# Performance work log

Hardware: AMD Instinct MI355X
Metric: run time of the kernel (lower is better)

The kernel has to match this reference:

```python
import jax, jax.numpy as jnp
import numpy as np

HIDDEN = 2048
NUM_HEADS = 16
HEAD_DIM = HIDDEN // NUM_HEADS
INTER = 8192
EPS = 1e-6


def setup_inputs() -> dict:
    key = jax.random.key(0)
    ks = jax.random.split(key, 10)
    s = 0.02
    return {
        "x": jax.random.normal(ks[0], (2, 2048, HIDDEN), dtype=jnp.float32),
        "w_ln1": jnp.ones((HIDDEN,), dtype=jnp.float32),
        "wq": jax.random.normal(ks[1], (HIDDEN, HIDDEN), dtype=jnp.float32) * s,
        "wk": jax.random.normal(ks[2], (HIDDEN, HIDDEN), dtype=jnp.float32) * s,
        "wv": jax.random.normal(ks[3], (HIDDEN, HIDDEN), dtype=jnp.float32) * s,
        "wo": jax.random.normal(ks[4], (HIDDEN, HIDDEN), dtype=jnp.float32) * s,
        "w_ln2": jnp.ones((HIDDEN,), dtype=jnp.float32),
        "wg": jax.random.normal(ks[5], (INTER, HIDDEN), dtype=jnp.float32) * s,
        "wu": jax.random.normal(ks[6], (INTER, HIDDEN), dtype=jnp.float32) * s,
        "wd": jax.random.normal(ks[7], (HIDDEN, INTER), dtype=jnp.float32) * s,
    }


def rmsnorm(x, w):
    rms = jnp.sqrt(jnp.mean(x * x, axis=-1, keepdims=True) + EPS)
    return x / rms * w


def attention(x, wq, wk, wv, wo):
    B, T, C = x.shape
    # weights are [out, in] (torch Linear convention) -> x @ W.T
    q = (x @ wq.T).reshape(B, T, NUM_HEADS, HEAD_DIM)
    k = (x @ wk.T).reshape(B, T, NUM_HEADS, HEAD_DIM)
    v = (x @ wv.T).reshape(B, T, NUM_HEADS, HEAD_DIM)
    scores = jnp.einsum("bqhd,bkhd->bhqk", q, k) / jnp.sqrt(jnp.float32(HEAD_DIM))
    attn = jax.nn.softmax(scores, axis=-1)
    out = jnp.einsum("bhqk,bkhd->bqhd", attn, v).reshape(B, T, C)
    return out @ wo.T


def mlp(x, wg, wu, wd):
    return (jax.nn.silu(x @ wg.T) * (x @ wu.T)) @ wd.T


def reference(x, w_ln1, wq, wk, wv, wo, w_ln2, wg, wu, wd):
    x = x + attention(rmsnorm(x, w_ln1), wq, wk, wv, wo)
    x = x + mlp(rmsnorm(x, w_ln2), wg, wu, wd)
    return x
```

## Files before the change

### kernel.cpp

```cpp
#include <hip/hip_runtime.h>
#include <stdint.h>

typedef unsigned short u16;
typedef unsigned int   u32;
typedef short s16x8 __attribute__((ext_vector_type(8)));
typedef u16   u16x8 __attribute__((ext_vector_type(8)));
typedef u32   u32x4 __attribute__((ext_vector_type(4)));
typedef float f32x4 __attribute__((ext_vector_type(4)));

__device__ __forceinline__ u16 f2bf(float f) {
    u32 u = __float_as_uint(f);
    u32 r = u + 0x7fffu + ((u >> 16) & 1u);
    return (u16)(r >> 16);
}
__device__ __forceinline__ float bf2f(u16 h) {
    return __uint_as_float(((u32)h) << 16);
}

__device__ __forceinline__ u32 cvtpk(float a, float b) {
    u32 r;
    asm("v_cvt_pk_bf16_f32 %0, %1, %2" : "=v"(r) : "v"(a), "v"(b));
    return r;
}
__device__ __forceinline__ void swap32(u32& a, u32& b) {
#if __has_builtin(__builtin_amdgcn_permlane32_swap)
    auto r = __builtin_amdgcn_permlane32_swap(a, b, false, false);
    a = r[0]; b = r[1];
#else
    asm volatile("v_permlane32_swap_b32 %0, %1" : "+v"(a), "+v"(b));
#endif
}
__device__ __forceinline__ void swap16(u32& a, u32& b) {
#if __has_builtin(__builtin_amdgcn_permlane16_swap)
    auto r = __builtin_amdgcn_permlane16_swap(a, b, false, false);
    a = r[0]; b = r[1];
#else
    asm volatile("v_permlane16_swap_b32 %0, %1" : "+v"(a), "+v"(b));
#endif
}

#define GLD16(gp, lp) __builtin_amdgcn_global_load_lds(                          \
    (const __attribute__((address_space(1))) void*)(uintptr_t)(gp),             \
    (__attribute__((address_space(3))) void*)(u32)(uintptr_t)(lp), 16, 0, 0)

#define FENCE asm volatile("" ::: "memory")

template<int N> __device__ __forceinline__ void waitv() {
    if constexpr (N == 0)      asm volatile("s_waitcnt vmcnt(0)" ::: "memory");
    else if constexpr (N == 2) asm volatile("s_waitcnt vmcnt(2)" ::: "memory");
    else if constexpr (N == 3) asm volatile("s_waitcnt vmcnt(3)" ::: "memory");
    else                       asm volatile("s_waitcnt vmcnt(4)" ::: "memory");
}

__global__ __launch_bounds__(256)
void cast_w(const float* __restrict__ in, u16* __restrict__ out, int n)
{
    const int i = (blockIdx.x * 256 + threadIdx.x) * 8;
    if (i >= n) return;
    f32x4 a = *(const f32x4*)(in + i);
    f32x4 b = *(const f32x4*)(in + i + 4);
    u16x8 o;
    o[0] = f2bf(a[0]); o[1] = f2bf(a[1]); o[2] = f2bf(a[2]); o[3] = f2bf(a[3]);
    o[4] = f2bf(b[0]); o[5] = f2bf(b[1]); o[6] = f2bf(b[2]); o[7] = f2bf(b[3]);
    *(u16x8*)(out + i) = o;
}

__global__ __launch_bounds__(256)
void rmsnorm_k(const float* __restrict__ x, const float* __restrict__ wln,
               u16* __restrict__ out, int C)
{
    const int row = blockIdx.x;
    const int tid = threadIdx.x;
    const float* xr = x + (size_t)row * C;
    f32x4 a = *(const f32x4*)(xr + tid * 8);
    f32x4 b = *(const f32x4*)(xr + tid * 8 + 4);
    float s = a[0]*a[0] + a[1]*a[1] + a[2]*a[2] + a[3]*a[3]
            + b[0]*b[0] + b[1]*b[1] + b[2]*b[2] + b[3]*b[3];
    #pragma unroll
    for (int off = 1; off < 64; off <<= 1) s += __shfl_xor(s, off);
    __shared__ float red[4];
    if ((tid & 63) == 0) red[tid >> 6] = s;
    __syncthreads();
    float tot = red[0] + red[1] + red[2] + red[3];
    float inv = rsqrtf(tot / (float)C + 1e-6f);
    f32x4 wa = *(const f32x4*)(wln + tid * 8);
    f32x4 wb = *(const f32x4*)(wln + tid * 8 + 4);
    u16x8 o;
    o[0] = f2bf(a[0]*inv*wa[0]); o[1] = f2bf(a[1]*inv*wa[1]);
    o[2] = f2bf(a[2]*inv*wa[2]); o[3] = f2bf(a[3]*inv*wa[3]);
    o[4] = f2bf(b[0]*inv*wb[0]); o[5] = f2bf(b[1]*inv*wb[1]);
    o[6] = f2bf(b[2]*inv*wb[2]); o[7] = f2bf(b[3]*inv*wb[3]);
    *(u16x8*)(out + (size_t)row * C + tid * 8) = o;
}

template<int MODE, int MR>
__global__ __launch_bounds__(512, 1)
void gemm8(const u16* __restrict__ A, const u16* __restrict__ W,
           const float* __restrict__ resid, const u16* __restrict__ aux,
           void* __restrict__ Cout, int M, int N, int K, float scale)
{
    constexpr int BM  = MR * 32;
    constexpr int MR2 = MR / 2;
    constexpr int SRA = MR * 8;
    constexpr int AL  = BM / 128;
    __shared__ __align__(16) u16 lds[2][(BM + 256) * 64];

    const int tid  = threadIdx.x;
    const int lane = tid & 63;
    const int w    = tid >> 6;
    const int wm   = w >> 2;
    const int wn   = w & 3;

    const int gx  = N >> 8;
    const int nwg = gridDim.x;
    const int sid = ((int)blockIdx.x & 7) * (nwg >> 3) + ((int)blockIdx.x >> 3);
    const int brow = (sid / gx) * BM;
    const int bcol = (sid % gx) * 256;

    const int KT = K >> 6;
    const int NI = KT >> 1;

    f32x4 acc[MR][4] = {};

    auto stageA = [&](int buf, int g, int kt) {
        #pragma unroll
        for (int j = 0; j < AL; ++j) {
            const int p   = j * 64 + (tid >> 3);
            const int row = ((p & ~(SRA - 1)) << 1) | (g * SRA) | (p & (SRA - 1));
            const int ch  = (tid & 7) ^ (row & 7);
            const u16* src = A + (size_t)(brow + row) * K + kt * 64 + ch * 8;
            const int p0  = j * 64 + (w << 3);
            const int r0  = ((p0 & ~(SRA - 1)) << 1) | (g * SRA) | (p0 & (SRA - 1));
            GLD16(src, &lds[buf][0] + r0 * 64);
        }
    };
    auto stageB = [&](int buf, int g, int kt) {
        #pragma unroll
        for (int j = 0; j < 2; ++j) {
            const int p   = j * 64 + (tid >> 3);
            const int row = ((p & ~31) << 1) | (g * 32) | (p & 31);
            const int ch  = (tid & 7) ^ (row & 7);
            const u16* src = W + (size_t)(bcol + row) * K + kt * 64 + ch * 8;
            const int p0  = j * 64 + (w << 3);
            const int r0  = ((p0 & ~31) << 1) | (g * 32) | (p0 & 31);
            GLD16(src, &lds[buf][BM * 64] + r0 * 64);
        }
    };

#define LDAF(AF, MH, BUF)                                                        \
    _Pragma("unroll") for (int f = 0; f < MR2; ++f)                              \
    _Pragma("unroll") for (int ks = 0; ks < 2; ++ks) {                           \
        const int row = wm * (BM / 2) + (MH) * (BM / 4) + f * 16 + (lane & 15);  \
        const int ch  = (ks * 4 + (lane >> 4)) ^ (row & 7);                      \
        AF[f][ks] = *(const s16x8*)(&lds[BUF][0] + row * 64 + ch * 8);           \
    }
#define LDBF(BQ, NH, BUF)                                                        \
    _Pragma("unroll") for (int g = 0; g < 2; ++g)                                \
    _Pragma("unroll") for (int ks = 0; ks < 2; ++ks) {                           \
        const int row = wn * 64 + (NH) * 32 + g * 16 + (lane & 15);              \
        const int ch  = (ks * 4 + (lane >> 4)) ^ (row & 7);                      \
        BQ[g][ks] = *(const s16x8*)(&lds[BUF][BM * 64] + row * 64 + ch * 8);     \
    }
#define MFQ(AF, BQ, MH, NH)                                                      \
    __builtin_amdgcn_s_setprio(1);                                               \
    _Pragma("unroll") for (int f = 0; f < MR2; ++f)                              \
    _Pragma("unroll") for (int g = 0; g < 2; ++g)                                \
    _Pragma("unroll") for (int ks = 0; ks < 2; ++ks)                             \
        acc[(MH) * MR2 + f][(NH) * 2 + g] =                                      \
            __builtin_amdgcn_mfma_f32_16x16x32_bf16(                             \
                AF[f][ks], BQ[g][ks], acc[(MH) * MR2 + f][(NH) * 2 + g], 0, 0, 0); \
    __builtin_amdgcn_s_setprio(0);
#define PH_ENTRY FENCE; __builtin_amdgcn_s_barrier();                            \
    asm volatile("s_waitcnt lgkmcnt(0)" ::: "memory"); FENCE

    s16x8 af[MR2][2], bqA[2][2], bqB[2][2];

    stageB(0, 0, 0); stageA(0, 0, 0); stageB(0, 1, 0); stageA(0, 1, 0);
    stageB(1, 0, 1); stageA(1, 0, 1); stageB(1, 1, 1);
    waitv<0>();
    FENCE; __builtin_amdgcn_s_barrier(); FENCE;
    LDAF(af, 0, 0) LDBF(bqA, 0, 0)

    for (int it = 0; it < NI; ++it) {
        const int t1  = 2 * it + 1;
        const int t0n = 2 * it + 2;
        const int t1n = 2 * it + 3;
        const bool last = (it == NI - 1);

        PH_ENTRY; MFQ(af, bqA, 0, 0)
        LDBF(bqB, 1, 0)
        stageA(1, 1, t1);
        PH_ENTRY; MFQ(af, bqB, 0, 1)
        LDAF(af, 1, 0)
        if (!last) stageB(0, 0, t0n);
        PH_ENTRY; MFQ(af, bqB, 1, 1)
        if (!last) stageA(0, 0, t0n);
        PH_ENTRY; MFQ(af, bqA, 1, 0)
        if (!last) stageB(0, 1, t0n);
        if (last) { waitv<0>(); } else { waitv<2>(); }
        LDAF(af, 0, 1) LDBF(bqA, 0, 1)
        PH_ENTRY; MFQ(af, bqA, 0, 0)
        LDBF(bqB, 1, 1)
        if (!last) stageA(0, 1, t0n);
        PH_ENTRY; MFQ(af, bqB, 0, 1)
        LDAF(af, 1, 1)
        if (!last) stageB(1, 0, t1n);
        PH_ENTRY; MFQ(af, bqB, 1, 1)
        if (!last) stageA(1, 0, t1n);
        PH_ENTRY; MFQ(af, bqA, 1, 0)
        if (!last) {
            stageB(1, 1, t1n);
            waitv<2>();
            LDAF(af, 0, 0) LDBF(bqA, 0, 0)
        }
    }
#undef LDAF
#undef LDBF
#undef MFQ
#undef PH_ENTRY

    const int er = (lane >> 4) * 4;
    const int ec = lane & 15;
    #pragma unroll
    for (int i = 0; i < MR; ++i) {
        #pragma unroll
        for (int j = 0; j < 4; ++j) {
            #pragma unroll
            for (int r = 0; r < 4; ++r) {
                const int row = brow + wm * (BM / 2) + i * 16 + er + r;
                const int col = bcol + wn * 64 + j * 16 + ec;
                const size_t idx = (size_t)row * N + col;
                const float va = acc[i][j][r];
                if (MODE == 0)      ((u16*)Cout)[idx] = f2bf(va);
                else if (MODE == 1) ((u16*)Cout)[idx] = f2bf(va * scale);
                else if (MODE == 2) ((float*)Cout)[idx] = resid[idx] + va;
                else {
                    const float g  = bf2f(aux[idx]);
                    const float sg = g / (1.0f + exp2f(-g * 1.4426950408889634f));
                    ((u16*)Cout)[idx] = f2bf(sg * va);
                }
            }
        }
    }
}

__global__ __launch_bounds__(256, 2)
void flash_attn(const u16* __restrict__ q, const u16* __restrict__ k,
                const u16* __restrict__ vT, u16* __restrict__ o)
{
    __shared__ __align__(16) u16 Kt[2][64 * 128];
    __shared__ __align__(16) u16 Vt[2][128 * 64];
    const int tid  = threadIdx.x;
    const int lane = tid & 63;
    const int w    = tid >> 6;
    const int qtile = blockIdx.x;
    const int bh    = blockIdx.y;
    const int b = bh >> 4, h = bh & 15;
    const size_t head  = ((size_t)b * 2048) * 2048 + (size_t)h * 128;
    const size_t vbase = ((size_t)h * 128) * 4096 + (size_t)b * 2048;

    s16x8 qf[2][4];
    #pragma unroll
    for (int qi = 0; qi < 2; ++qi) {
        const int tq = qtile * 128 + w * 32 + qi * 16 + (lane & 15);
        const u16* qp = q + head + (size_t)tq * 2048 + (lane >> 4) * 8;
        #pragma unroll
        for (int dk = 0; dk < 4; ++dk) qf[qi][dk] = *(const s16x8*)(qp + dk * 32);
    }

    f32x4 oa[2][8] = {};
    float m_r[2] = {-1e30f, -1e30f};
    float l_r[2] = {0.f, 0.f};

    const int krow = tid >> 2;
    const int kc0  = (tid & 3) * 32;
    const int vd   = tid >> 1;
    const int vk0  = (tid & 1) * 32;
    const u16* kg = k + head + (size_t)krow * 2048 + kc0;
    const u16* vg = vT + vbase + (size_t)vd * 4096 + vk0;
    u32 kwo[4], vwo[4];
    #pragma unroll
    for (int c = 0; c < 4; ++c) {
        kwo[c] = (u32)((krow * 256 + (kc0 + c * 8) * 2) ^ ((krow & 7) << 4));
        vwo[c] = (u32)((vd * 128 + (vk0 + c * 8) * 2)   ^ ((vd & 7) << 4));
    }

    s16x8 kr[4], vr[4];
    #pragma unroll
    for (int c = 0; c < 4; ++c) {
        kr[c] = *(const s16x8*)(kg + c * 8);
        vr[c] = *(const s16x8*)(vg + c * 8);
    }

    for (int kb = 0; kb < 32; ++kb) {
        const int cur = kb & 1;
        char* KtB = (char*)&Kt[cur][0];
        char* VtB = (char*)&Vt[cur][0];
        #pragma unroll
        for (int c = 0; c < 4; ++c) {
            *(s16x8*)(KtB + kwo[c]) = kr[c];
            *(s16x8*)(VtB + vwo[c]) = vr[c];
        }
        if (kb + 1 < 32) {
            const int k0n = (kb + 1) * 64;
            #pragma unroll
            for (int c = 0; c < 4; ++c) {
                kr[c] = *(const s16x8*)(kg + (size_t)k0n * 2048 + c * 8);
                vr[c] = *(const s16x8*)(vg + k0n + c * 8);
            }
        }
        asm volatile("s_waitcnt lgkmcnt(0)" ::: "memory");
        __builtin_amdgcn_s_barrier();
        FENCE;

        f32x4 st[2][4] = {};
        __builtin_amdgcn_s_setprio(1);
        #pragma unroll
        for (int kt = 0; kt < 4; ++kt) {
            const int row = kt * 16 + (lane & 15);
            s16x8 kf[4];
            #pragma unroll
            for (int dk = 0; dk < 4; ++dk) {
                const int dcol = dk * 32 + (lane >> 4) * 8;
                kf[dk] = *(const s16x8*)(KtB + ((row * 256 + dcol * 2) ^ ((row & 7) << 4)));
            }
            #pragma unroll
            for (int qi = 0; qi < 2; ++qi)
                #pragma unroll
                for (int dk = 0; dk < 4; ++dk)
                    st[qi][kt] = __builtin_amdgcn_mfma_f32_16x16x32_bf16(kf[dk], qf[qi][dk], st[qi][kt], 0, 0, 0);
        }
        __builtin_amdgcn_s_setprio(0);

        float mx[2];
        #pragma unroll
        for (int qi = 0; qi < 2; ++qi) {
            float m0 = fmaxf(fmaxf(st[qi][0][0], st[qi][0][1]), fmaxf(st[qi][0][2], st[qi][0][3]));
            float m1 = fmaxf(fmaxf(st[qi][1][0], st[qi][1][1]), fmaxf(st[qi][1][2], st[qi][1][3]));
            float m2 = fmaxf(fmaxf(st[qi][2][0], st[qi][2][1]), fmaxf(st[qi][2][2], st[qi][2][3]));
            float m3 = fmaxf(fmaxf(st[qi][3][0], st[qi][3][1]), fmaxf(st[qi][3][2], st[qi][3][3]));
            float m0123 = fmaxf(fmaxf(m0, m1), fmaxf(m2, m3));
            m0123 = fmaxf(m0123, __shfl_xor(m0123, 16));
            m0123 = fmaxf(m0123, __shfl_xor(m0123, 32));
            mx[qi] = m0123;
        }
        const bool grow = (mx[0] > m_r[0] + 8.f) || (mx[1] > m_r[1] + 8.f);
        if (__any(grow)) {
            #pragma unroll
            for (int qi = 0; qi < 2; ++qi) {
                const float mn = fmaxf(m_r[qi], mx[qi]);
                const float sc = exp2f(m_r[qi] - mn);
                m_r[qi] = mn;
                l_r[qi] *= sc;
                const float s0 = __shfl(sc, (lane >> 4) * 4 + 0);
                const float s1 = __shfl(sc, (lane >> 4) * 4 + 1);
                const float s2 = __shfl(sc, (lane >> 4) * 4 + 2);
                const float s3 = __shfl(sc, (lane >> 4) * 4 + 3);
                #pragma unroll
                for (int ni = 0; ni < 8; ++ni) {
                    oa[qi][ni][0] *= s0; oa[qi][ni][1] *= s1;
                    oa[qi][ni][2] *= s2; oa[qi][ni][3] *= s3;
                }
            }
        }

        s16x8 pa[2][2];
        #pragma unroll
        for (int qi = 0; qi < 2; ++qi) {
            float sum = 0.f;
            #pragma unroll
            for (int kt = 0; kt < 4; ++kt)
                #pragma unroll
                for (int r = 0; r < 4; ++r) {
                    const float p = exp2f(st[qi][kt][r] - m_r[qi]);
                    st[qi][kt][r] = p;
                    sum += p;
                }
            sum += __shfl_xor(sum, 16);
            sum += __shfl_xor(sum, 32);
            l_r[qi] += sum;

            u32 q01[4], q23[4];
            #pragma unroll
            for (int kt = 0; kt < 4; ++kt) {
                q01[kt] = cvtpk(st[qi][kt][0], st[qi][kt][1]);
                q23[kt] = cvtpk(st[qi][kt][2], st[qi][kt][3]);
            }
            #pragma unroll
            for (int ks = 0; ks < 2; ++ks) {
                u32 X = q01[2 * ks], Y = q01[2 * ks + 1];
                swap32(X, Y); swap16(X, Y);
                u32 U = q23[2 * ks], V = q23[2 * ks + 1];
                swap32(U, V); swap16(U, V);
                u32x4 t; t[0] = X; t[1] = U; t[2] = Y; t[3] = V;
                pa[qi][ks] = __builtin_bit_cast(s16x8, t);
            }
        }

        __builtin_amdgcn_s_setprio(1);
        #pragma unroll
        for (int ks = 0; ks < 2; ++ks) {
            const int keyb = ks * 32 + (lane >> 4) * 8;
            #pragma unroll
            for (int ni = 0; ni < 8; ++ni) {
                const int dd = ni * 16 + (lane & 15);
                s16x8 vf = *(const s16x8*)(VtB + ((dd * 128 + keyb * 2) ^ ((dd & 7) << 4)));
                #pragma unroll
                for (int qi = 0; qi < 2; ++qi)
                    oa[qi][ni] = __builtin_amdgcn_mfma_f32_16x16x32_bf16(pa[qi][ks], vf, oa[qi][ni], 0, 0, 0);
            }
        }
        __builtin_amdgcn_s_setprio(0);
    }
    #pragma unroll
    for (int qi = 0; qi < 2; ++qi) {
        #pragma unroll
        for (int r = 0; r < 4; ++r) {
            const float inv = 1.0f / __shfl(l_r[qi], (lane >> 4) * 4 + r);
            const int tout = qtile * 128 + w * 32 + qi * 16 + (lane >> 4) * 4 + r;
            u16* op = o + head + (size_t)tout * 2048 + (lane & 15);
            #pragma unroll
            for (int ni = 0; ni < 8; ++ni)
                op[ni * 16] = f2bf(oa[qi][ni][r] * inv);
        }
    }
}

extern "C" void kernel_launch(void* const* d_in, const int* in_sizes, int n_in,
                              void* d_out, int out_size, void* d_ws, size_t ws_size,
                              hipStream_t stream)
{
    (void)in_sizes; (void)n_in; (void)out_size; (void)ws_size;
    const float* x    = (const float*)d_in[0];
    const float* wln1 = (const float*)d_in[1];
    const float* wq   = (const float*)d_in[2];
    const float* wk   = (const float*)d_in[3];
    const float* wv   = (const float*)d_in[4];
    const float* wo   = (const float*)d_in[5];
    const float* wln2 = (const float*)d_in[6];
    const float* wg   = (const float*)d_in[7];
    const float* wu   = (const float*)d_in[8];
    const float* wd   = (const float*)d_in[9];
    float* out = (float*)d_out;

    const size_t MB = 1024ull * 1024ull;
    char* ws = (char*)d_ws;
    u16*   arena = (u16*)(ws + 0);
    float* hbuf  = (float*)(ws + 32 * MB);
    u16*   xn    = (u16*)(ws + 64 * MB);
    u16*   qb    = (u16*)(ws + 80 * MB);
    u16*   kbuf  = (u16*)(ws + 96 * MB);
    u16*   vT    = (u16*)(ws + 112 * MB);
    u16*   abuf  = (u16*)(ws + 128 * MB);
    u16*   gbuf  = (u16*)(ws + 80 * MB);

    const int M = 4096, C = 2048, I = 8192;
    const float qscale = 0.1275164899f;
    dim3 blk(256);
    dim3 blk8(512);

    rmsnorm_k<<<M, blk, 0, stream>>>(x, wln1, xn, C);

    cast_w<<<(C * C) / 2048, blk, 0, stream>>>(wq, arena, C * C);
    gemm8<1, 4><<<dim3((C / 256) * (M / 128)), blk8, 0, stream>>>(xn, arena, nullptr, nullptr, qb, M, C, C, qscale);
    cast_w<<<(C * C) / 2048, blk, 0, stream>>>(wk, arena, C * C);
    gemm8<0, 4><<<dim3((C / 256) * (M / 128)), blk8, 0, stream>>>(xn, arena, nullptr, nullptr, kbuf, M, C, C, 1.f);
    cast_w<<<(C * C) / 2048, blk, 0, stream>>>(wv, arena, C * C);
    gemm8<0, 4><<<dim3((M / 256) * (C / 128)), blk8, 0, stream>>>(arena, xn, nullptr, nullptr, vT, C, M, C, 1.f);

    flash_attn<<<dim3(2048 / 128, 32), blk, 0, stream>>>(qb, kbuf, vT, abuf);

    cast_w<<<(C * C) / 2048, blk, 0, stream>>>(wo, arena, C * C);
    gemm8<2, 4><<<dim3((C / 256) * (M / 128)), blk8, 0, stream>>>(abuf, arena, x, nullptr, hbuf, M, C, C, 1.f);

    rmsnorm_k<<<M, blk, 0, stream>>>(hbuf, wln2, xn, C);

    cast_w<<<(I * C) / 2048, blk, 0, stream>>>(wg, arena, I * C);
    gemm8<0, 8><<<dim3((I / 256) * (M / 256)), blk8, 0, stream>>>(xn, arena, nullptr, nullptr, gbuf, M, I, C, 1.f);
    cast_w<<<(I * C) / 2048, blk, 0, stream>>>(wu, arena, I * C);
    gemm8<3, 8><<<dim3((I / 256) * (M / 256)), blk8, 0, stream>>>(xn, arena, nullptr, gbuf, gbuf, M, I, C, 1.f);
    cast_w<<<(C * I) / 2048, blk, 0, stream>>>(wd, arena, C * I);
    gemm8<2, 4><<<dim3((C / 256) * (M / 128)), blk8, 0, stream>>>(gbuf, arena, hbuf, nullptr, out, M, C, I, 1.f);
}
```

Measured before the change: 717.9 us.

## Add 256-thread 256x256 GEMM kernel and fuse Q/K projections

Adds a new GEMM kernel where each workgroup has 4 waves and a 256x256 output tile. Each wave computes a 128x128 sub-tile with 32x32x16 bf16 MFMA and keeps a double-buffered LDS pipeline that issues the next stage's loads in the middle of the compute. The new kernel replaces the 512-thread gemm8 for the gate and up MLP projections. The Q and K weights are now cast into adjacent arena regions so one launch computes both, and the epilogue writes columns below 2048 scaled to Q and the rest to K. The aim is more operand reuse per wave and fewer launches, in exchange for higher register pressure (a 4x4 grid of f32x16 accumulators) and uncoalesced scalar epilogue stores.

```diff
diff --git a/kernel.cpp b/kernel.cpp
--- a/kernel.cpp
+++ b/kernel.cpp
@@ -7,6 +7,7 @@
 typedef u16   u16x8 __attribute__((ext_vector_type(8)));
 typedef u32   u32x4 __attribute__((ext_vector_type(4)));
 typedef float f32x4 __attribute__((ext_vector_type(4)));
+typedef float f32x16 __attribute__((ext_vector_type(16)));
 
 __device__ __forceinline__ u16 f2bf(float f) {
     u32 u = __float_as_uint(f);
@@ -46,10 +47,11 @@
 #define FENCE asm volatile("" ::: "memory")
 
 template<int N> __device__ __forceinline__ void waitv() {
-    if constexpr (N == 0)      asm volatile("s_waitcnt vmcnt(0)" ::: "memory");
-    else if constexpr (N == 2) asm volatile("s_waitcnt vmcnt(2)" ::: "memory");
-    else if constexpr (N == 3) asm volatile("s_waitcnt vmcnt(3)" ::: "memory");
-    else                       asm volatile("s_waitcnt vmcnt(4)" ::: "memory");
+    if constexpr (N == 0)       asm volatile("s_waitcnt vmcnt(0)" ::: "memory");
+    else if constexpr (N == 2)  asm volatile("s_waitcnt vmcnt(2)" ::: "memory");
+    else if constexpr (N == 3)  asm volatile("s_waitcnt vmcnt(3)" ::: "memory");
+    else if constexpr (N == 16) asm volatile("s_waitcnt vmcnt(16)" ::: "memory");
+    else                        asm volatile("s_waitcnt vmcnt(4)" ::: "memory");
 }
 
 __global__ __launch_bounds__(256)
@@ -93,6 +95,139 @@
     *(u16x8*)(out + (size_t)row * C + tid * 8) = o;
 }
 
+template<int MODE>
+__global__ __launch_bounds__(256, 1)
+void gemm32(const u16* __restrict__ A, const u16* __restrict__ W,
+            const float* __restrict__ resid, const u16* __restrict__ aux,
+            void* __restrict__ Cout, int M, int N, int K, float scale)
+{
+    __shared__ __align__(16) u16 lds[2][512 * 64];
+
+    const int tid  = threadIdx.x;
+    const int lane = tid & 63;
+    const int w    = tid >> 6;
+    const int wm   = w >> 1;
+    const int wn   = w & 1;
+
+    const int gx  = N >> 8;
+    const int nwg = gridDim.x;
+    const int sid = ((int)blockIdx.x & 7) * (nwg >> 3) + ((int)blockIdx.x >> 3);
+    const int brow = (sid / gx) * 256;
+    const int bcol = (sid % gx) * 256;
+
+    const int KT = K >> 6;
+
+    f32x16 acc[4][4] = {};
+
+    auto stage = [&](int buf, int kt) {
+        #pragma unroll
+        for (int j = 0; j < 8; ++j) {
+            const int row = j * 32 + (tid >> 3);
+            const int ch  = (tid & 7) ^ (row & 7);
+            GLD16(A + (size_t)(brow + row) * K + kt * 64 + ch * 8,
+                  &lds[buf][0] + (j * 32 + w * 8) * 64);
+        }
+        #pragma unroll
+        for (int j = 0; j < 8; ++j) {
+            const int row = j * 32 + (tid >> 3);
+            const int ch  = (tid & 7) ^ (row & 7);
+            GLD16(W + (size_t)(bcol + row) * K + kt * 64 + ch * 8,
+                  &lds[buf][512 * 32] + (j * 32 + w * 8) * 64);
+        }
+    };
+
+    stage(0, 0);
+    stage(1, 1);
+    waitv<16>();
+    FENCE; __builtin_amdgcn_s_barrier(); FENCE;
+
+    for (int t = 0; t < KT; ++t) {
+        const int cur = t & 1;
+        const u16* Ab = &lds[cur][0];
+        const u16* Bb = &lds[cur][512 * 32];
+
+        s16x8 af[4][4], bq[4][4];
+        #pragma unroll
+        for (int i = 0; i < 4; ++i)
+            #pragma unroll
+            for (int ks = 0; ks < 4; ++ks) {
+                const int row = wm * 128 + i * 32 + (lane & 31);
+                const int ch  = (ks * 2 + (lane >> 5)) ^ (row & 7);
+                af[i][ks] = *(const s16x8*)(Ab + row * 64 + ch * 8);
+            }
+        #pragma unroll
+        for (int j = 0; j < 4; ++j)
+            #pragma unroll
+            for (int ks = 0; ks < 4; ++ks) {
+                const int row = wn * 128 + j * 32 + (lane & 31);
+                const int ch  = (ks * 2 + (lane >> 5)) ^ (row & 7);
+                bq[j][ks] = *(const s16x8*)(Bb + row * 64 + ch * 8);
+            }
+
+        __builtin_amdgcn_s_setprio(1);
+        #pragma unroll
+        for (int i = 0; i < 4; ++i)
+            #pragma unroll
+            for (int j = 0; j < 2; ++j)
+                #pragma unroll
+                for (int ks = 0; ks < 4; ++ks)
+                    acc[i][j] = __builtin_amdgcn_mfma_f32_32x32x16_bf16(
+                        af[i][ks], bq[j][ks], acc[i][j], 0, 0, 0);
+        __builtin_amdgcn_s_setprio(0);
+
+        asm volatile("s_waitcnt lgkmcnt(0)" ::: "memory");
+        FENCE; __builtin_amdgcn_s_barrier(); FENCE;
+        if (t + 2 < KT) stage(cur, t + 2);
+
+        __builtin_amdgcn_s_setprio(1);
+        #pragma unroll
+        for (int i = 0; i < 4; ++i)
+            #pragma unroll
+            for (int j = 2; j < 4; ++j)
+                #pragma unroll
+                for (int ks = 0; ks < 4; ++ks)
+                    acc[i][j] = __builtin_amdgcn_mfma_f32_32x32x16_bf16(
+                        af[i][ks], bq[j][ks], acc[i][j], 0, 0, 0);
+        __builtin_amdgcn_s_setprio(0);
+
+        if (t + 1 < KT) {
+            if (t + 2 < KT) waitv<16>(); else waitv<0>();
+            FENCE; __builtin_amdgcn_s_barrier(); FENCE;
+        }
+    }
+
+    const int cl = lane & 31;
+    const int rh = 4 * (lane >> 5);
+    #pragma unroll
+    for (int i = 0; i < 4; ++i) {
+        #pragma unroll
+        for (int j = 0; j < 4; ++j) {
+            #pragma unroll
+            for (int r = 0; r < 16; ++r) {
+                const int row = brow + wm * 128 + i * 32 + (r & 3) + 8 * (r >> 2) + rh;
+                const int col = bcol + wn * 128 + j * 32 + cl;
+                const float va = acc[i][j][r];
+                if (MODE == 0) {
+                    ((u16*)Cout)[(size_t)row * N + col] = f2bf(va);
+                } else if (MODE == 2) {
+                    const size_t idx = (size_t)row * N + col;
+                    ((float*)Cout)[idx] = resid[idx] + va;
+                } else if (MODE == 3) {
+                    const size_t idx = (size_t)row * N + col;
+                    const float g  = bf2f(aux[idx]);
+                    const float sg = g / (1.0f + exp2f(-g * 1.4426950408889634f));
+                    ((u16*)Cout)[idx] = f2bf(sg * va);
+                } else {
+                    if (col < 2048)
+                        ((u16*)Cout)[(size_t)row * 2048 + col] = f2bf(va * scale);
+                    else
+                        ((u16*)aux)[(size_t)row * 2048 + (col - 2048)] = f2bf(va);
+                }
+            }
+        }
+    }
+}
+
 template<int MODE, int MR>
 __global__ __launch_bounds__(512, 1)
 void gemm8(const u16* __restrict__ A, const u16* __restrict__ W,
@@ -462,9 +597,10 @@
     rmsnorm_k<<<M, blk, 0, stream>>>(x, wln1, xn, C);
 
     cast_w<<<(C * C) / 2048, blk, 0, stream>>>(wq, arena, C * C);
-    gemm8<1, 4><<<dim3((C / 256) * (M / 128)), blk8, 0, stream>>>(xn, arena, nullptr, nullptr, qb, M, C, C, qscale);
-    cast_w<<<(C * C) / 2048, blk, 0, stream>>>(wk, arena, C * C);
-    gemm8<0, 4><<<dim3((C / 256) * (M / 128)), blk8, 0, stream>>>(xn, arena, nullptr, nullptr, kbuf, M, C, C, 1.f);
+    cast_w<<<(C * C) / 2048, blk, 0, stream>>>(wk, arena + (size_t)C * C, C * C);
+    gemm32<4><<<dim3((2 * C / 256) * (M / 256)), blk, 0, stream>>>(
+        xn, arena, nullptr, kbuf, qb, M, 2 * C, C, qscale);
+
     cast_w<<<(C * C) / 2048, blk, 0, stream>>>(wv, arena, C * C);
     gemm8<0, 4><<<dim3((M / 256) * (C / 128)), blk8, 0, stream>>>(arena, xn, nullptr, nullptr, vT, C, M, C, 1.f);
 
@@ -476,9 +612,9 @@
     rmsnorm_k<<<M, blk, 0, stream>>>(hbuf, wln2, xn, C);
 
     cast_w<<<(I * C) / 2048, blk, 0, stream>>>(wg, arena, I * C);
-    gemm8<0, 8><<<dim3((I / 256) * (M / 256)), blk8, 0, stream>>>(xn, arena, nullptr, nullptr, gbuf, M, I, C, 1.f);
+    gemm32<0><<<dim3((I / 256) * (M / 256)), blk, 0, stream>>>(xn, arena, nullptr, nullptr, gbuf, M, I, C, 1.f);
     cast_w<<<(I * C) / 2048, blk, 0, stream>>>(wu, arena, I * C);
-    gemm8<3, 8><<<dim3((I / 256) * (M / 256)), blk8, 0, stream>>>(xn, arena, nullptr, gbuf, gbuf, M, I, C, 1.f);
+    gemm32<3><<<dim3((I / 256) * (M / 256)), blk, 0, stream>>>(xn, arena, nullptr, gbuf, gbuf, M, I, C, 1.f);
     cast_w<<<(C * I) / 2048, blk, 0, stream>>>(wd, arena, C * I);
     gemm8<2, 4><<<dim3((C / 256) * (M / 128)), blk8, 0, stream>>>(gbuf, arena, hbuf, nullptr, out, M, C, I, 1.f);
 }
```

Measured after the change: 882.3 us. 22.9% more time.
